# Kernel tuning notes

Hardware: AMD Instinct MI355X
Metric: run time of the kernel (lower is better)

The kernel has to match this reference:

```python
import jax, jax.numpy as jnp
import numpy as np

NUM_GRAPHS = 2048  # graph.batch_size
EPS = 1e-6


def setup_inputs() -> dict:
    key = jax.random.key(0)
    k1, k2 = jax.random.split(key)
    N, D = 1000000, 128
    feat = jax.random.normal(k1, (N, D), dtype=jnp.float32)
    segment_ids = jnp.sort(jax.random.randint(k2, (N,), 0, NUM_GRAPHS)).astype(jnp.int64)
    weight = jnp.ones((D,), dtype=jnp.float32)
    bias = jnp.zeros((D,), dtype=jnp.float32)
    mean_scale = jnp.ones((D,), dtype=jnp.float32)
    return {"feat": feat, "segment_ids": segment_ids, "weight": weight,
            "bias": bias, "mean_scale": mean_scale}


def reference(feat, segment_ids, weight, bias, mean_scale):
    # counts per graph ( == graph.batch_num_nodes() ). Clamp to 1 so that
    # empty segments (which never contribute to the output) don't produce NaNs.
    counts = jnp.maximum(
        jax.ops.segment_sum(jnp.ones_like(segment_ids, dtype=feat.dtype),
                            segment_ids, num_segments=NUM_GRAPHS), 1.0)
    inv_counts = (1.0 / counts)[:, None]                      # [B, 1]

    # per-graph mean: scatter_add then divide by segment size
    mean = jax.ops.segment_sum(feat, segment_ids, num_segments=NUM_GRAPHS) * inv_counts  # [B, D]
    sub = feat - mean[segment_ids] * mean_scale               # [N, D]

    # per-graph std of the mean-shifted features
    var = jax.ops.segment_sum(sub * sub, segment_ids, num_segments=NUM_GRAPHS) * inv_counts
    std = jnp.sqrt(var + EPS)                                 # [B, D]

    return weight * sub / std[segment_ids] + bias
```

## Files before the change

kernel.cpp:

```cpp
#include <hip/hip_runtime.h>

#define D 128
#define NSEG 2048
#define EPSV 1e-6f
#define BLOCK 512
#define QCH 8
#define NQ 4
#define CPRF 32
#define RG (BLOCK/QCH)
#define WAVES (BLOCK/64)
#define MAXK 8

typedef float f32x4 __attribute__((ext_vector_type(4)));

__global__ void seg_bounds(const int* __restrict__ seg, int* __restrict__ offs, int N) {
    const int i = blockIdx.x * blockDim.x + threadIdx.x;
    if (i <= NSEG) {
        int lo = 0, hi = N;
        while (lo < hi) {
            int mid = (lo + hi) >> 1;
            if (seg[mid] < i) lo = mid + 1; else hi = mid;
        }
        offs[i] = lo;
    }
}

__global__ __launch_bounds__(BLOCK, 6) void graphnorm_fused(
    const float* __restrict__ feat,
    const int* __restrict__ offs,
    const float* __restrict__ weight,
    const float* __restrict__ bias,
    const float* __restrict__ mean_scale,
    float* __restrict__ out)
{
    const int bid = blockIdx.x;
    const int s = bid >> 2;
    const int q = bid & 3;

    const int start = offs[s];
    const int end   = offs[s + 1];

    const int t = threadIdx.x;
    const int c = t & (QCH - 1);
    const int g = t >> 3;
    const int chunk = q * QCH + c;

    __shared__ f32x4 s_sum[WAVES][QCH];
    __shared__ f32x4 s_sq[WAVES][QCH];

    const f32x4* feat4 = reinterpret_cast<const f32x4*>(feat);
    f32x4* out4 = reinterpret_cast<f32x4*>(out);

    f32x4 buf[MAXK];
    #pragma unroll
    for (int k = 0; k < MAXK; ++k) {
        const int r = start + g + k * RG;
        if (r < end) buf[k] = feat4[r * CPRF + chunk];
    }

    f32x4 s0 = 0.f, q0 = 0.f;
    #pragma unroll
    for (int k = 0; k < MAXK; ++k) {
        const int r = start + g + k * RG;
        if (r < end) {
            s0 += buf[k];
            q0 += buf[k] * buf[k];
        }
    }

    const int tail_base = start + g + MAXK * RG;
    for (int r = tail_base; r < end; r += RG) {
        f32x4 v = feat4[r * CPRF + chunk];
        s0 += v;
        q0 += v * v;
    }

    #pragma unroll
    for (int i = 0; i < 4; ++i) {
        s0[i] += __shfl_xor(s0[i], 8);
        s0[i] += __shfl_xor(s0[i], 16);
        s0[i] += __shfl_xor(s0[i], 32);
        q0[i] += __shfl_xor(q0[i], 8);
        q0[i] += __shfl_xor(q0[i], 16);
        q0[i] += __shfl_xor(q0[i], 32);
    }

    const int w    = t >> 6;
    const int lane = t & 63;
    if (lane < QCH) {
        s_sum[w][lane] = s0;
        s_sq[w][lane]  = q0;
    }
    __syncthreads();

    f32x4 sm = s_sum[0][c];
    f32x4 sg = s_sq[0][c];
    #pragma unroll
    for (int i = 1; i < WAVES; ++i) {
        sm += s_sum[i][c];
        sg += s_sq[i][c];
    }
    const float cnt = (float)max(end - start, 1);
    const float inv = 1.0f / cnt;
    const f32x4 wv  = reinterpret_cast<const f32x4*>(weight)[chunk];
    const f32x4 bi  = reinterpret_cast<const f32x4*>(bias)[chunk];
    const f32x4 msc = reinterpret_cast<const f32x4*>(mean_scale)[chunk];
    f32x4 A, B;
    #pragma unroll
    for (int i = 0; i < 4; ++i) {
        float mean = sm[i] * inv;
        float ms   = mean * msc[i];
        float var  = fmaxf(sg[i] * inv - 2.f * mean * ms + ms * ms, 0.f);
        float istd = rsqrtf(var + EPSV);
        A[i] = wv[i] * istd;
        B[i] = bi[i] - A[i] * ms;
    }

    #pragma unroll
    for (int k = 0; k < MAXK; ++k) {
        const int r = start + g + k * RG;
        if (r < end)
            __builtin_nontemporal_store(A * buf[k] + B, &out4[r * CPRF + chunk]);
    }
    for (int r = tail_base; r < end; r += RG) {
        f32x4 v = feat4[r * CPRF + chunk];
        __builtin_nontemporal_store(A * v + B, &out4[r * CPRF + chunk]);
    }
}

extern "C" void kernel_launch(void* const* d_in, const int* in_sizes, int n_in,
                              void* d_out, int out_size, void* d_ws, size_t ws_size,
                              hipStream_t stream) {
    const float* feat       = (const float*)d_in[0];
    const int*   seg        = (const int*)d_in[1];
    const float* weight     = (const float*)d_in[2];
    const float* bias       = (const float*)d_in[3];
    const float* mean_scale = (const float*)d_in[4];
    float* out = (float*)d_out;
    int* offs  = (int*)d_ws;

    const int N = in_sizes[0] / D;

    seg_bounds<<<(NSEG + 1 + 255) / 256, 256, 0, stream>>>(seg, offs, N);
    graphnorm_fused<<<NSEG * NQ, BLOCK, 0, stream>>>(
        feat, offs, weight, bias, mean_scale, out);
}
```

Measured before the change: 203.6 us.

## Convert graph-norm kernel to persistent blocks with double-buffered tile prefetch

Replaces the one-block-per-(segment, quarter) launch with 512 persistent blocks that each walk 16 consecutive tiles. The kernel holds two register buffers and shared-memory partial-sum slots, loading the next tile's features while the current tile is reduced and written out, with an explicit LDS wait and barrier. The aim is to hide global-load latency and cut block launch overhead. The cost is higher register pressure (launch bounds lowered to 4), and with only 512 blocks there are about two blocks per CU, which reduces occupancy in a kernel that is already close to bandwidth-bound.

```diff
diff --git a/kernel.cpp b/kernel.cpp
--- a/kernel.cpp
+++ b/kernel.cpp
@@ -10,6 +10,8 @@
 #define RG (BLOCK/QCH)
 #define WAVES (BLOCK/64)
 #define MAXK 8
+#define TILES 16
+#define NBLK (NSEG*NQ/TILES)
 
 typedef float f32x4 __attribute__((ext_vector_type(4)));
 
@@ -25,7 +27,7 @@
     }
 }
 
-__global__ __launch_bounds__(BLOCK, 6) void graphnorm_fused(
+__global__ __launch_bounds__(BLOCK, 4) void graphnorm_persist(
     const float* __restrict__ feat,
     const int* __restrict__ offs,
     const float* __restrict__ weight,
@@ -33,98 +35,115 @@
     const float* __restrict__ mean_scale,
     float* __restrict__ out)
 {
-    const int bid = blockIdx.x;
-    const int s = bid >> 2;
-    const int q = bid & 3;
+    const int t = threadIdx.x;
+    const int c    = t & (QCH - 1);
+    const int g    = t >> 3;
+    const int w    = t >> 6;
+    const int lane = t & 63;
 
-    const int start = offs[s];
-    const int end   = offs[s + 1];
-
-    const int t = threadIdx.x;
-    const int c = t & (QCH - 1);
-    const int g = t >> 3;
-    const int chunk = q * QCH + c;
-
-    __shared__ f32x4 s_sum[WAVES][QCH];
-    __shared__ f32x4 s_sq[WAVES][QCH];
+    __shared__ f32x4 p_sum[2][WAVES][QCH];
+    __shared__ f32x4 p_sq[2][WAVES][QCH];
 
     const f32x4* feat4 = reinterpret_cast<const f32x4*>(feat);
     f32x4* out4 = reinterpret_cast<f32x4*>(out);
+    const int base = blockIdx.x * TILES;
 
-    f32x4 buf[MAXK];
-    #pragma unroll
-    for (int k = 0; k < MAXK; ++k) {
-        const int r = start + g + k * RG;
-        if (r < end) buf[k] = feat4[r * CPRF + chunk];
+    f32x4 bufA[MAXK], bufB[MAXK];
+    int stA, enA, chA, stB, enB, chB;
+
+#define TILEINFO(TI, ST, EN, CH)                 \
+    {                                            \
+        const int s_ = (TI) >> 2;                \
+        ST = offs[s_];                           \
+        EN = offs[s_ + 1];                       \
+        CH = ((TI) & 3) * QCH + c;               \
     }
 
-    f32x4 s0 = 0.f, q0 = 0.f;
-    #pragma unroll
-    for (int k = 0; k < MAXK; ++k) {
-        const int r = start + g + k * RG;
-        if (r < end) {
-            s0 += buf[k];
-            q0 += buf[k] * buf[k];
-        }
+#define STAGE(BUF, ST, EN, CH)                           \
+    _Pragma("unroll")                                    \
+    for (int k = 0; k < MAXK; ++k) {                     \
+        const int r = ST + g + k * RG;                   \
+        if (r < EN) BUF[k] = feat4[r * CPRF + CH];       \
     }
 
-    const int tail_base = start + g + MAXK * RG;
-    for (int r = tail_base; r < end; r += RG) {
-        f32x4 v = feat4[r * CPRF + chunk];
-        s0 += v;
-        q0 += v * v;
+#define CONSUME(BUF, ST, EN, CH, P)                                        \
+    {                                                                      \
+        f32x4 s0 = 0.f, q0 = 0.f;                                          \
+        _Pragma("unroll")                                                  \
+        for (int k = 0; k < MAXK; ++k) {                                   \
+            const int r = ST + g + k * RG;                                 \
+            if (r < EN) { s0 += BUF[k]; q0 += BUF[k] * BUF[k]; }           \
+        }                                                                  \
+        const int tail_base = ST + g + MAXK * RG;                          \
+        for (int r = tail_base; r < EN; r += RG) {                         \
+            f32x4 v = feat4[r * CPRF + CH];                                \
+            s0 += v; q0 += v * v;                                          \
+        }                                                                  \
+        _Pragma("unroll")                                                  \
+        for (int i = 0; i < 4; ++i) {                                      \
+            s0[i] += __shfl_xor(s0[i], 8);                                 \
+            s0[i] += __shfl_xor(s0[i], 16);                                \
+            s0[i] += __shfl_xor(s0[i], 32);                                \
+            q0[i] += __shfl_xor(q0[i], 8);                                 \
+            q0[i] += __shfl_xor(q0[i], 16);                                \
+            q0[i] += __shfl_xor(q0[i], 32);                                \
+        }                                                                  \
+        if (lane < QCH) {                                                  \
+            p_sum[P][w][lane] = s0;                                        \
+            p_sq[P][w][lane]  = q0;                                        \
+        }                                                                  \
+        asm volatile("s_waitcnt lgkmcnt(0)" ::: "memory");                 \
+        __builtin_amdgcn_s_barrier();                                      \
+        __builtin_amdgcn_sched_barrier(0);                                 \
+        f32x4 sm = p_sum[P][0][c];                                         \
+        f32x4 sg = p_sq[P][0][c];                                          \
+        _Pragma("unroll")                                                  \
+        for (int i = 1; i < WAVES; ++i) {                                  \
+            sm += p_sum[P][i][c];                                          \
+            sg += p_sq[P][i][c];                                           \
+        }                                                                  \
+        const float cnt = (float)max(EN - ST, 1);                          \
+        const float inv = 1.0f / cnt;                                      \
+        const f32x4 wv  = reinterpret_cast<const f32x4*>(weight)[CH];      \
+        const f32x4 bi  = reinterpret_cast<const f32x4*>(bias)[CH];        \
+        const f32x4 msc = reinterpret_cast<const f32x4*>(mean_scale)[CH];  \
+        f32x4 Aa, Bb;                                                      \
+        _Pragma("unroll")                                                  \
+        for (int i = 0; i < 4; ++i) {                                      \
+            float mean = sm[i] * inv;                                      \
+            float ms   = mean * msc[i];                                    \
+            float var  = fmaxf(sg[i] * inv - 2.f * mean * ms + ms * ms, 0.f); \
+            float istd = rsqrtf(var + EPSV);                               \
+            Aa[i] = wv[i] * istd;                                          \
+            Bb[i] = bi[i] - Aa[i] * ms;                                    \
+        }                                                                  \
+        _Pragma("unroll")                                                  \
+        for (int k = 0; k < MAXK; ++k) {                                   \
+            const int r = ST + g + k * RG;                                 \
+            if (r < EN)                                                    \
+                __builtin_nontemporal_store(Aa * BUF[k] + Bb,              \
+                                            &out4[r * CPRF + CH]);         \
+        }                                                                  \
+        for (int r = tail_base; r < EN; r += RG) {                         \
+            f32x4 v = feat4[r * CPRF + CH];                                \
+            __builtin_nontemporal_store(Aa * v + Bb, &out4[r * CPRF + CH]);\
+        }                                                                  \
     }
 
-    #pragma unroll
-    for (int i = 0; i < 4; ++i) {
-        s0[i] += __shfl_xor(s0[i], 8);
-        s0[i] += __shfl_xor(s0[i], 16);
-        s0[i] += __shfl_xor(s0[i], 32);
-        q0[i] += __shfl_xor(q0[i], 8);
-        q0[i] += __shfl_xor(q0[i], 16);
-        q0[i] += __shfl_xor(q0[i], 32);
-    }
+    TILEINFO(base, stA, enA, chA);
+    STAGE(bufA, stA, enA, chA);
 
-    const int w    = t >> 6;
-    const int lane = t & 63;
-    if (lane < QCH) {
-        s_sum[w][lane] = s0;
-        s_sq[w][lane]  = q0;
-    }
-    __syncthreads();
+    #pragma unroll 1
+    for (int it = 0; it < TILES; it += 2) {
+        TILEINFO(base + it + 1, stB, enB, chB);
+        STAGE(bufB, stB, enB, chB);
+        CONSUME(bufA, stA, enA, chA, 0);
 
-    f32x4 sm = s_sum[0][c];
-    f32x4 sg = s_sq[0][c];
-    #pragma unroll
-    for (int i = 1; i < WAVES; ++i) {
-        sm += s_sum[i][c];
-        sg += s_sq[i][c];
-    }
-    const float cnt = (float)max(end - start, 1);
-    const float inv = 1.0f / cnt;
-    const f32x4 wv  = reinterpret_cast<const f32x4*>(weight)[chunk];
-    const f32x4 bi  = reinterpret_cast<const f32x4*>(bias)[chunk];
-    const f32x4 msc = reinterpret_cast<const f32x4*>(mean_scale)[chunk];
-    f32x4 A, B;
-    #pragma unroll
-    for (int i = 0; i < 4; ++i) {
-        float mean = sm[i] * inv;
-        float ms   = mean * msc[i];
-        float var  = fmaxf(sg[i] * inv - 2.f * mean * ms + ms * ms, 0.f);
-        float istd = rsqrtf(var + EPSV);
-        A[i] = wv[i] * istd;
-        B[i] = bi[i] - A[i] * ms;
-    }
-
-    #pragma unroll
-    for (int k = 0; k < MAXK; ++k) {
-        const int r = start + g + k * RG;
-        if (r < end)
-            __builtin_nontemporal_store(A * buf[k] + B, &out4[r * CPRF + chunk]);
-    }
-    for (int r = tail_base; r < end; r += RG) {
-        f32x4 v = feat4[r * CPRF + chunk];
-        __builtin_nontemporal_store(A * v + B, &out4[r * CPRF + chunk]);
+        if (it + 2 < TILES) {
+            TILEINFO(base + it + 2, stA, enA, chA);
+            STAGE(bufA, stA, enA, chA);
+        }
+        CONSUME(bufB, stB, enB, chB, 1);
     }
 }
 
@@ -142,6 +161,6 @@
     const int N = in_sizes[0] / D;
 
     seg_bounds<<<(NSEG + 1 + 255) / 256, 256, 0, stream>>>(seg, offs, N);
-    graphnorm_fused<<<NSEG * NQ, BLOCK, 0, stream>>>(
+    graphnorm_persist<<<NBLK, BLOCK, 0, stream>>>(
         feat, offs, weight, bias, mean_scale, out);
 }
```

Result: slower. 212.3 us (+4.3%).
